# Optimization experiments

Measured on AMD Instinct MI355X. Metric: run time of the kernel, lower is better.

## Reference

```python
import jax, jax.numpy as jnp
import numpy as np
import math

N_NODES = 100000
N_EDGES = 1600000
IN_CH = 128
EDGE_DIM = 8
HEADS = 4
C1, C2 = 10, 5  # per-head out channels of conv1/conv2
N_GRAPHS = 64


def setup_inputs() -> dict:
    key = jax.random.key(0)
    k = jax.random.split(key, 26)
    s = 0.05
    d1, d2 = HEADS * C1, HEADS * C2  # 40, 20
    lin = lambda kk, fi, fo: jax.random.normal(kk, (fi, fo), jnp.float32) * s
    inp = {}
    inp['x'] = jax.random.normal(k[0], (N_NODES, IN_CH), jnp.float32)
    inp['edge_index'] = jax.random.randint(k[1], (2, N_EDGES), 0, N_NODES)
    inp['edge_attr'] = jax.random.normal(k[2], (N_EDGES, EDGE_DIM), jnp.float32)
    inp['batch'] = jnp.sort(jax.random.randint(k[3], (N_NODES,), 0, N_GRAPHS))
    # conv1 params (TransformerConv: lin_query/key/value + lin_edge(no bias) + lin_skip)
    inp['Wq1'] = lin(k[4], IN_CH, d1); inp['bq1'] = jnp.zeros((d1,), jnp.float32)
    inp['Wk1'] = lin(k[5], IN_CH, d1); inp['bk1'] = jnp.zeros((d1,), jnp.float32)
    inp['Wv1'] = lin(k[6], IN_CH, d1); inp['bv1'] = jnp.zeros((d1,), jnp.float32)
    inp['We1'] = lin(k[7], EDGE_DIM, d1)
    inp['Ws1'] = lin(k[8], IN_CH, d1); inp['bs1'] = jnp.zeros((d1,), jnp.float32)
    # conv2 params
    inp['Wq2'] = lin(k[9], d1, d2); inp['bq2'] = jnp.zeros((d2,), jnp.float32)
    inp['Wk2'] = lin(k[10], d1, d2); inp['bk2'] = jnp.zeros((d2,), jnp.float32)
    inp['Wv2'] = lin(k[11], d1, d2); inp['bv2'] = jnp.zeros((d2,), jnp.float32)
    inp['We2'] = lin(k[12], EDGE_DIM, d2)
    inp['Ws2'] = lin(k[13], d1, d2); inp['bs2'] = jnp.zeros((d2,), jnp.float32)
    # MLP head
    inp['W1'] = lin(k[14], d2, 10); inp['b1'] = jnp.zeros((10,), jnp.float32)
    inp['W2'] = lin(k[15], 10, 3); inp['b2'] = jnp.zeros((3,), jnp.float32)
    return inp


def _segment_softmax(alpha, dst, n):
    # numerically stable softmax over incoming edges of each target node
    amax = jax.ops.segment_max(alpha, dst, num_segments=n)
    ex = jnp.exp(alpha - amax[dst])
    den = jax.ops.segment_sum(ex, dst, num_segments=n)
    return ex / (den[dst] + 1e-16)


def _transformer_conv(x, src, dst, eattr, Wq, bq, Wk, bk, Wv, bv, We, Ws, bs, heads, ch):
    n = x.shape[0]
    q = (x @ Wq + bq).reshape(n, heads, ch)
    k = (x @ Wk + bk).reshape(n, heads, ch)
    v = (x @ Wv + bv).reshape(n, heads, ch)
    e = (eattr @ We).reshape(-1, heads, ch)          # [E,H,C]
    kj = k[src] + e                                   # gather + edge bias
    alpha = jnp.einsum('ehc,ehc->eh', q[dst], kj) / math.sqrt(ch)
    alpha = _segment_softmax(alpha, dst, n)           # [E,H]
    msg = (v[src] + e) * alpha[:, :, None]
    out = jax.ops.segment_sum(msg, dst, num_segments=n).reshape(n, heads * ch)
    return out + x @ Ws + bs                          # root/skip connection (beta=False)


def reference(x, edge_index, edge_attr, batch, Wq1, bq1, Wk1, bk1, Wv1, bv1, We1, Ws1, bs1, Wq2, bq2, Wk2, bk2, Wv2, bv2, We2, Ws2, bs2, W1, b1, W2, b2):
    src, dst = edge_index[0], edge_index[1]
    h = jax.nn.relu(_transformer_conv(x, src, dst, edge_attr, Wq1, bq1, Wk1, bk1, Wv1, bv1, We1, Ws1, bs1, HEADS, C1))
    h = jax.nn.relu(_transformer_conv(h, src, dst, edge_attr, Wq2, bq2, Wk2, bk2, Wv2, bv2, We2, Ws2, bs2, HEADS, C2))
    # global_mean_pool
    sums = jax.ops.segment_sum(h, batch, num_segments=N_GRAPHS)
    cnt = jax.ops.segment_sum(jnp.ones((h.shape[0],), h.dtype), batch, num_segments=N_GRAPHS)
    pooled = sums / jnp.maximum(cnt, 1.0)[:, None]
    h = jax.nn.relu(pooled @ W1 + b1)
    return h @ W2 + b2
```

## Files before the change

### kernel.cpp

```cpp
#include <hip/hip_runtime.h>
#include <math.h>

__device__ __forceinline__ unsigned bfr_(float f) {
    unsigned u = __float_as_uint(f);
    return (u + 0x7fffu + ((u >> 16) & 1u)) >> 16;
}
__device__ __forceinline__ unsigned pack2_(float lo, float hi) {
    return bfr_(lo) | (bfr_(hi) << 16);
}
__device__ __forceinline__ float unlo_(unsigned u) { return __uint_as_float(u << 16); }
__device__ __forceinline__ float unhi_(unsigned u) { return __uint_as_float(u & 0xffff0000u); }
__device__ __forceinline__ float bf2f_(unsigned short us) {
    return __uint_as_float((unsigned)us << 16);
}

__global__ void k_hist(const int* __restrict__ dst, int* __restrict__ deg, int E) {
    int e = blockIdx.x * 256 + threadIdx.x;
    if (e < E) atomicAdd(&deg[dst[e]], 1);
}

__global__ void k_scan1(const int* __restrict__ deg, int* __restrict__ rp,
                        int* __restrict__ bsum, int n) {
    __shared__ int sh[256];
    int t = threadIdx.x;
    int base = blockIdx.x * 1024 + t * 4;
    int v0 = (base + 0 < n) ? deg[base + 0] : 0;
    int v1 = (base + 1 < n) ? deg[base + 1] : 0;
    int v2 = (base + 2 < n) ? deg[base + 2] : 0;
    int v3 = (base + 3 < n) ? deg[base + 3] : 0;
    int ts = v0 + v1 + v2 + v3;
    sh[t] = ts;
    __syncthreads();
    for (int off = 1; off < 256; off <<= 1) {
        int x = (t >= off) ? sh[t - off] : 0;
        __syncthreads();
        sh[t] += x;
        __syncthreads();
    }
    int run = sh[t] - ts;
    if (base + 0 < n) rp[base + 0] = run;
    run += v0;
    if (base + 1 < n) rp[base + 1] = run;
    run += v1;
    if (base + 2 < n) rp[base + 2] = run;
    run += v2;
    if (base + 3 < n) rp[base + 3] = run;
    if (t == 255) bsum[blockIdx.x] = sh[255];
}

__global__ void k_scan2(int* __restrict__ bsum, int nb) {
    __shared__ int sh[256];
    int t = threadIdx.x;
    int v = (t < nb) ? bsum[t] : 0;
    sh[t] = v;
    __syncthreads();
    for (int off = 1; off < 256; off <<= 1) {
        int x = (t >= off) ? sh[t - off] : 0;
        __syncthreads();
        sh[t] += x;
        __syncthreads();
    }
    if (t < nb) bsum[t] = sh[t] - v;
}

__global__ void k_scan3(int* __restrict__ rp, const int* __restrict__ bsum,
                        int* __restrict__ cur, int n, int total) {
    int t = threadIdx.x;
    int base = blockIdx.x * 1024 + t * 4;
    int add = bsum[blockIdx.x];
    if (base + 0 < n) { rp[base + 0] += add; cur[base + 0] = 0; }
    if (base + 1 < n) { rp[base + 1] += add; cur[base + 1] = 0; }
    if (base + 2 < n) { rp[base + 2] += add; cur[base + 2] = 0; }
    if (base + 3 < n) { rp[base + 3] += add; cur[base + 3] = 0; }
    if (blockIdx.x == 0 && t == 0) rp[n] = total;
}

__global__ void k_scatter(const int* __restrict__ src, const int* __restrict__ dst,
                          const int* __restrict__ rp, int* __restrict__ cur,
                          const float4* __restrict__ ea, int* __restrict__ src_perm,
                          uint4* __restrict__ eap, int E) {
    int e = blockIdx.x * 256 + threadIdx.x;
    if (e >= E) return;
    float4 a = ea[(size_t)e * 2 + 0];
    float4 b = ea[(size_t)e * 2 + 1];
    uint4 u;
    u.x = pack2_(a.x, a.y);
    u.y = pack2_(a.z, a.w);
    u.z = pack2_(b.x, b.y);
    u.w = pack2_(b.z, b.w);
    int d = dst[e];
    int pos = rp[d] + atomicAdd(&cur[d], 1);
    src_perm[pos] = src[e];
    eap[pos] = u;
}

template <int FIN, int CH, int KTILE, int NPT, int CHPAD, int NPB>
__global__ __launch_bounds__(256) void k_proj(
    const float* __restrict__ X,
    const float* __restrict__ Wq, const float* __restrict__ Wk,
    const float* __restrict__ Wv, const float* __restrict__ Ws,
    const float* __restrict__ bq, const float* __restrict__ bk,
    const float* __restrict__ bv, const float* __restrict__ bs,
    float* __restrict__ qO, unsigned* __restrict__ kvO,
    unsigned short* __restrict__ sO, int N) {
    constexpr int FOUT = 4 * CH;
    constexpr int STRIDE = 4 * CHPAD;
    constexpr int COLS = 4 * FOUT;
    constexpr int NCG = COLS / 10;
    constexpr int NG = 256 / NCG;
    static_assert(NG * NPT == NPB, "geometry");
    constexpr int F4 = FIN / 4;
    __shared__ float xs[FIN * NPB];
    __shared__ float wbuf[KTILE * COLS];
    int t = threadIdx.x;
    int nb = blockIdx.x * NPB;
    for (int i = t; i < NPB * F4; i += 256) {
        int nl = i % NPB;
        int k4 = (i / NPB) * 4;
        int node = nb + nl;
        float4 val = make_float4(0.f, 0.f, 0.f, 0.f);
        if (node < N) val = *(const float4*)(X + (size_t)node * FIN + k4);
        xs[(k4 + 0) * NPB + nl] = val.x;
        xs[(k4 + 1) * NPB + nl] = val.y;
        xs[(k4 + 2) * NPB + nl] = val.z;
        xs[(k4 + 3) * NPB + nl] = val.w;
    }
    int cg = t % NCG, ng = t / NCG;
    int which = (cg * 10) / FOUT, cc0 = (cg * 10) % FOUT;
    float acc[NPT][10];
#pragma unroll
    for (int i = 0; i < NPT; ++i)
#pragma unroll
        for (int j = 0; j < 10; ++j) acc[i][j] = 0.f;

    for (int kt = 0; kt < FIN; kt += KTILE) {
        __syncthreads();
        for (int i = t; i < KTILE * (COLS / 4); i += 256) {
            int kk = i / (COLS / 4);
            int c4 = (i % (COLS / 4)) * 4;
            int wh = c4 / FOUT, cc = c4 % FOUT;
            const float* Wsrc = wh == 0 ? Wq : wh == 1 ? Wk : wh == 2 ? Wv : Ws;
            float4 wv = *(const float4*)(Wsrc + (size_t)(kt + kk) * FOUT + cc);
            wbuf[kk * COLS + c4 + 0] = wv.x;
            wbuf[kk * COLS + c4 + 1] = wv.y;
            wbuf[kk * COLS + c4 + 2] = wv.z;
            wbuf[kk * COLS + c4 + 3] = wv.w;
        }
        __syncthreads();
#pragma unroll 4
        for (int kk = 0; kk < KTILE; ++kk) {
            float xv[NPT];
            if constexpr (NPT == 4) {
                float4 x4 = *(const float4*)(xs + (kt + kk) * NPB + ng * 4);
                xv[0] = x4.x; xv[1] = x4.y; xv[2] = x4.z; xv[3] = x4.w;
            } else if constexpr (NPT == 2) {
                float2 x2 = *(const float2*)(xs + (kt + kk) * NPB + ng * 2);
                xv[0] = x2.x; xv[1] = x2.y;
            } else {
                xv[0] = xs[(kt + kk) * NPB + ng];
            }
            const float2* wp = (const float2*)(wbuf + kk * COLS + cg * 10);
            float wv[10];
#pragma unroll
            for (int jj = 0; jj < 5; ++jj) {
                float2 w2 = wp[jj];
                wv[2 * jj] = w2.x;
                wv[2 * jj + 1] = w2.y;
            }
#pragma unroll
            for (int i = 0; i < NPT; ++i)
#pragma unroll
                for (int j = 0; j < 10; ++j) acc[i][j] += xv[i] * wv[j];
        }
    }
    const float* B = which == 0 ? bq : which == 1 ? bk : which == 2 ? bv : bs;
    float bias[10];
#pragma unroll
    for (int j = 0; j < 10; ++j) bias[j] = B[cc0 + j];
    __syncthreads();
    if (which == 0) {
#pragma unroll
        for (int i = 0; i < NPT; ++i) {
            int node = nb + ng * NPT + i;
            if (node < N)
#pragma unroll
                for (int j = 0; j < 10; ++j) {
                    int col = cc0 + j, hh = col / CH, cc = col % CH;
                    qO[(size_t)node * STRIDE + hh * CHPAD + cc] = acc[i][j] + bias[j];
                }
        }
    } else if (which == 3) {
#pragma unroll
        for (int i = 0; i < NPT; ++i) {
            int node = nb + ng * NPT + i;
            if (node < N)
#pragma unroll
                for (int j = 0; j < 10; ++j)
                    sO[(size_t)node * FOUT + cc0 + j] =
                        (unsigned short)bfr_(acc[i][j] + bias[j]);
        }
    } else if (which == 1) {
#pragma unroll
        for (int i = 0; i < NPT; ++i) {
            int nl = ng * NPT + i;
#pragma unroll
            for (int j = 0; j < 10; ++j) wbuf[nl * FOUT + cc0 + j] = acc[i][j] + bias[j];
        }
    }
    __syncthreads();
    if (which == 2) {
#pragma unroll
        for (int i = 0; i < NPT; ++i) {
            int nl = ng * NPT + i;
            int node = nb + nl;
            if (node < N)
#pragma unroll
                for (int j = 0; j < 10; ++j) {
                    int col = cc0 + j, hh = col / CH, cc = col % CH;
                    float kf = wbuf[nl * FOUT + cc0 + j];
                    kvO[(size_t)node * STRIDE + hh * CHPAD + cc] =
                        pack2_(kf, acc[i][j] + bias[j]);
                }
        }
    }
}

template <int CH, int CHPAD, bool SHIFT>
__global__ __launch_bounds__(256) void k_conv(
    const int* __restrict__ rp, const int* __restrict__ src_perm,
    const uint4* __restrict__ eap, const float* __restrict__ We,
    const float* __restrict__ q, const unsigned* __restrict__ kv,
    const unsigned short* __restrict__ skp, float* __restrict__ hout,
    float inv_sqrt, int N) {
    constexpr int D = 4 * CH;
    constexpr int STRIDE = 4 * CHPAD;
    constexpr int RAWN = SHIFT ? CHPAD + 2 : CHPAD;
    constexpr int NLD = RAWN / 4;
    __shared__ float we_s[8 * D];
    for (int i = threadIdx.x; i < 8 * D; i += 256) we_s[i] = We[i];
    __syncthreads();
    int g = blockIdx.x * 256 + threadIdx.x;
    int node = g >> 4;
    int h = g & 3;
    int qtr = (g >> 2) & 3;
    if (node >= N) return;
    int start_off = SHIFT ? ((h * CH) & ~3) : h * CHPAD;
    int rs = rp[node], re = rp[node + 1];
    float qh[CH];
    {
        float qraw[RAWN];
        const float4* qp = (const float4*)(q + (size_t)node * STRIDE + start_off);
#pragma unroll
        for (int i = 0; i < NLD; ++i) *(float4*)&qraw[4 * i] = qp[i];
        if constexpr (SHIFT) {
            if (h & 1) {
#pragma unroll
                for (int c = 0; c < CH; ++c) qraw[c] = qraw[c + 2];
            }
        }
#pragma unroll
        for (int c = 0; c < CH; ++c) qh[c] = qraw[c];
    }
    float qe[8];
#pragma unroll
    for (int j = 0; j < 8; ++j) {
        float sE = 0.f;
#pragma unroll
        for (int c = 0; c < CH; ++c) sE += qh[c] * we_s[j * D + h * CH + c];
        qe[j] = sE;
    }
    float m = -3.0e38f, l = 0.f;
    float accv[CH] = {};
    float acce[8] = {};
    for (int p = rs + qtr; p < re; p += 4) {
        int sidx = src_perm[p];
        uint4 eu = eap[p];
        float ea8[8];
        ea8[0] = unlo_(eu.x); ea8[1] = unhi_(eu.x);
        ea8[2] = unlo_(eu.y); ea8[3] = unhi_(eu.y);
        ea8[4] = unlo_(eu.z); ea8[5] = unhi_(eu.z);
        ea8[6] = unlo_(eu.w); ea8[7] = unhi_(eu.w);
        unsigned kraw[RAWN];
        const uint4* kp = (const uint4*)(kv + (size_t)sidx * STRIDE + start_off);
#pragma unroll
        for (int i = 0; i < NLD; ++i) *(uint4*)&kraw[4 * i] = kp[i];
        if constexpr (SHIFT) {
            if (h & 1) {
#pragma unroll
                for (int c = 0; c < CH; ++c) kraw[c] = kraw[c + 2];
            }
        }
        float a = 0.f;
        float vj[CH];
#pragma unroll
        for (int c = 0; c < CH; ++c) {
            unsigned u = kraw[c];
            a += qh[c] * unlo_(u);
            vj[c] = unhi_(u);
        }
#pragma unroll
        for (int j = 0; j < 8; ++j) a += qe[j] * ea8[j];
        a *= inv_sqrt;
        float mn = fmaxf(m, a);
        float so = __expf(m - mn);
        float w = __expf(a - mn);
        l = l * so + w;
#pragma unroll
        for (int c = 0; c < CH; ++c) accv[c] = accv[c] * so + w * vj[c];
#pragma unroll
        for (int j = 0; j < 8; ++j) acce[j] = acce[j] * so + w * ea8[j];
        m = mn;
    }
#pragma unroll
    for (int mask = 4; mask <= 8; mask <<= 1) {
        float mo = __shfl_xor(m, mask);
        float lo = __shfl_xor(l, mask);
        float mn = fmaxf(m, mo);
        float s1 = (m > -1e37f) ? __expf(m - mn) : 0.f;
        float s2 = (mo > -1e37f) ? __expf(mo - mn) : 0.f;
        l = l * s1 + lo * s2;
#pragma unroll
        for (int c = 0; c < CH; ++c) {
            float ao = __shfl_xor(accv[c], mask);
            accv[c] = accv[c] * s1 + ao * s2;
        }
#pragma unroll
        for (int j = 0; j < 8; ++j) {
            float ao = __shfl_xor(acce[j], mask);
            acce[j] = acce[j] * s1 + ao * s2;
        }
        m = mn;
    }
    if (qtr == 0) {
        float inv = 1.0f / (l + 1e-16f);
#pragma unroll
        for (int c = 0; c < CH; ++c) {
            float ec = 0.f;
#pragma unroll
            for (int j = 0; j < 8; ++j) ec += acce[j] * we_s[j * D + h * CH + c];
            float o = (accv[c] + ec) * inv + bf2f_(skp[(size_t)node * D + h * CH + c]);
            hout[(size_t)node * D + h * CH + c] = fmaxf(o, 0.f);
        }
    }
}

__global__ void k_pool(const float* __restrict__ h2, const int* __restrict__ batch,
                       float* __restrict__ pooled, float* __restrict__ cnt, int N) {
    int t = blockIdx.x * 256 + threadIdx.x;
    int start = t * 16;
    if (start >= N) return;
    int end = min(start + 16, N);
    float acc[20];
#pragma unroll
    for (int c = 0; c < 20; ++c) acc[c] = 0.f;
    int cg = batch[start];
    float run = 0.f;
    for (int n = start; n < end; ++n) {
        int g = batch[n];
        if (g != cg) {
#pragma unroll
            for (int c = 0; c < 20; ++c) atomicAdd(&pooled[cg * 20 + c], acc[c]);
            atomicAdd(&cnt[cg], run);
#pragma unroll
            for (int c = 0; c < 20; ++c) acc[c] = 0.f;
            run = 0.f;
            cg = g;
        }
#pragma unroll
        for (int c = 0; c < 20; ++c) acc[c] += h2[(size_t)n * 20 + c];
        run += 1.f;
    }
#pragma unroll
    for (int c = 0; c < 20; ++c) atomicAdd(&pooled[cg * 20 + c], acc[c]);
    atomicAdd(&cnt[cg], run);
}

__global__ void k_mlp(const float* __restrict__ pooled, const float* __restrict__ cnt,
                      const float* __restrict__ W1, const float* __restrict__ b1,
                      const float* __restrict__ W2, const float* __restrict__ b2,
                      float* __restrict__ out) {
    int g = threadIdx.x;
    if (g >= 64) return;
    float ic = 1.0f / fmaxf(cnt[g], 1.0f);
    float p[20];
#pragma unroll
    for (int i = 0; i < 20; ++i) p[i] = pooled[g * 20 + i] * ic;
    float hid[10];
#pragma unroll
    for (int j = 0; j < 10; ++j) {
        float a = b1[j];
#pragma unroll
        for (int i = 0; i < 20; ++i) a += p[i] * W1[i * 10 + j];
        hid[j] = fmaxf(a, 0.f);
    }
#pragma unroll
    for (int o = 0; o < 3; ++o) {
        float a = b2[o];
#pragma unroll
        for (int j = 0; j < 10; ++j) a += hid[j] * W2[j * 3 + o];
        out[g * 3 + o] = a;
    }
}

extern "C" void kernel_launch(void* const* d_in, const int* in_sizes, int n_in,
                              void* d_out, int out_size, void* d_ws, size_t ws_size,
                              hipStream_t stream) {
    const float* x   = (const float*)d_in[0];
    const int* ei    = (const int*)d_in[1];
    const float* ea  = (const float*)d_in[2];
    const int* batch = (const int*)d_in[3];
    const float *Wq1 = (const float*)d_in[4],  *bq1 = (const float*)d_in[5];
    const float *Wk1 = (const float*)d_in[6],  *bk1 = (const float*)d_in[7];
    const float *Wv1 = (const float*)d_in[8],  *bv1 = (const float*)d_in[9];
    const float *We1 = (const float*)d_in[10];
    const float *Ws1 = (const float*)d_in[11], *bs1 = (const float*)d_in[12];
    const float *Wq2 = (const float*)d_in[13], *bq2 = (const float*)d_in[14];
    const float *Wk2 = (const float*)d_in[15], *bk2 = (const float*)d_in[16];
    const float *Wv2 = (const float*)d_in[17], *bv2 = (const float*)d_in[18];
    const float *We2 = (const float*)d_in[19];
    const float *Ws2 = (const float*)d_in[20], *bs2 = (const float*)d_in[21];
    const float *W1  = (const float*)d_in[22], *b1  = (const float*)d_in[23];
    const float *W2  = (const float*)d_in[24], *b2  = (const float*)d_in[25];

    const int N = in_sizes[0] / 128;
    const int E = in_sizes[1] / 2;
    const int* srcI = ei;
    const int* dstI = ei + E;

    float* F = (float*)d_ws;
    float*          q    = F;
    unsigned*       kv   = (unsigned*)(F + 4000000);
    float*          h1   = F + 8000000;
    float*          h2   = F + 8000000;
    unsigned short* s_bf = (unsigned short*)(F + 12000000);
    uint4*          eap  = (uint4*)(F + 14000000);
    int*       src_perm  = (int*)(F + 20400000);
    int* I = (int*)(F + 22000000);
    int* deg  = I;
    int* cur  = I;
    int* rpR  = I + 100352;
    int* bsum = I + 200704;
    float* pooled = F + 22300000;
    float* cnt    = pooled + 1280;

    const int SCAN_BLOCKS = (N + 1023) / 1024;
    const int EB = (E + 255) / 256;

    hipMemsetAsync(deg, 0, (size_t)N * 4, stream);
    hipMemsetAsync(pooled, 0, (1280 + 64) * 4, stream);

    k_hist<<<EB, 256, 0, stream>>>(dstI, deg, E);
    k_scan1<<<SCAN_BLOCKS, 256, 0, stream>>>(deg, rpR, bsum, N);
    k_scan2<<<1, 256, 0, stream>>>(bsum, SCAN_BLOCKS);
    k_scan3<<<SCAN_BLOCKS, 256, 0, stream>>>(rpR, bsum, cur, N, E);
    k_scatter<<<EB, 256, 0, stream>>>(srcI, dstI, rpR, cur, (const float4*)ea,
                                      src_perm, eap, E);

    k_proj<128, 10, 8, 4, 10, 64><<<(N + 63) / 64, 256, 0, stream>>>(
        x, Wq1, Wk1, Wv1, Ws1, bq1, bk1, bv1, bs1, q, kv, s_bf, N);
    k_conv<10, 10, true><<<(16 * N + 255) / 256, 256, 0, stream>>>(
        rpR, src_perm, eap, We1, q, kv, s_bf, h1, 0.31622776601683794f, N);

    k_proj<40, 5, 40, 1, 8, 32><<<(N + 31) / 32, 256, 0, stream>>>(
        h1, Wq2, Wk2, Wv2, Ws2, bq2, bk2, bv2, bs2, q, kv, s_bf, N);
    k_conv<5, 8, false><<<(16 * N + 255) / 256, 256, 0, stream>>>(
        rpR, src_perm, eap, We2, q, kv, s_bf, h2, 0.4472135954999579f, N);

    k_pool<<<((N + 15) / 16 + 255) / 256, 256, 0, stream>>>(h2, batch, pooled, cnt, N);
    k_mlp<<<1, 64, 0, stream>>>(pooled, cnt, W1, b1, W2, b2, (float*)d_out);
}
```

Measured before the change: 524.1 us.

## Split CSR scatter into bucketed staging pass and per-bucket local scatter

Replaces the single per-edge CSR scatter with two passes. The first pass uses one atomic counter per bucket of 16 destination nodes to write packed 64-bit records (local dst, edge id, src) into a staging buffer. The second pass runs one block per bucket, assigns final positions with shared-memory atomics, and writes src_perm and the bf16-packed edge attributes. The aim is to localize the random writes of the 16-byte edge-attribute records and cut global atomic contention, at the cost of an extra staging write/read and a gather of edge attributes by id. Bit packing assumes src < 2^17 and edge id < 2^21, and the staging buffer aliases the q buffer.

```diff
diff --git a/kernel.cpp b/kernel.cpp
--- a/kernel.cpp
+++ b/kernel.cpp
@@ -64,34 +64,64 @@
 }
 
 __global__ void k_scan3(int* __restrict__ rp, const int* __restrict__ bsum,
-                        int* __restrict__ cur, int n, int total) {
+                        int* __restrict__ bcur, int n, int total, int nbk) {
     int t = threadIdx.x;
     int base = blockIdx.x * 1024 + t * 4;
     int add = bsum[blockIdx.x];
-    if (base + 0 < n) { rp[base + 0] += add; cur[base + 0] = 0; }
-    if (base + 1 < n) { rp[base + 1] += add; cur[base + 1] = 0; }
-    if (base + 2 < n) { rp[base + 2] += add; cur[base + 2] = 0; }
-    if (base + 3 < n) { rp[base + 3] += add; cur[base + 3] = 0; }
+    if (base + 0 < n) rp[base + 0] += add;
+    if (base + 1 < n) rp[base + 1] += add;
+    if (base + 2 < n) rp[base + 2] += add;
+    if (base + 3 < n) rp[base + 3] += add;
+    int gid = blockIdx.x * 256 + t;
+    if (gid < nbk) bcur[gid] = 0;
     if (blockIdx.x == 0 && t == 0) rp[n] = total;
 }
 
-__global__ void k_scatter(const int* __restrict__ src, const int* __restrict__ dst,
-                          const int* __restrict__ rp, int* __restrict__ cur,
-                          const float4* __restrict__ ea, int* __restrict__ src_perm,
-                          uint4* __restrict__ eap, int E) {
+__global__ void k_scatterB(const int* __restrict__ src, const int* __restrict__ dst,
+                           const int* __restrict__ rp, int* __restrict__ bcur,
+                           unsigned long long* __restrict__ staging, int E) {
     int e = blockIdx.x * 256 + threadIdx.x;
     if (e >= E) return;
-    float4 a = ea[(size_t)e * 2 + 0];
-    float4 b = ea[(size_t)e * 2 + 1];
-    uint4 u;
-    u.x = pack2_(a.x, a.y);
-    u.y = pack2_(a.z, a.w);
-    u.z = pack2_(b.x, b.y);
-    u.w = pack2_(b.z, b.w);
     int d = dst[e];
-    int pos = rp[d] + atomicAdd(&cur[d], 1);
-    src_perm[pos] = src[e];
-    eap[pos] = u;
+    int b = d >> 4;
+    int pos = rp[d & ~15] + atomicAdd(&bcur[b], 1);
+    unsigned long long rec = ((unsigned long long)(d & 15) << 38) |
+                             ((unsigned long long)(unsigned)e << 17) |
+                             (unsigned long long)(unsigned)src[e];
+    staging[pos] = rec;
+}
+
+__global__ __launch_bounds__(256) void k_scatterC(
+    const int* __restrict__ rp, const unsigned long long* __restrict__ staging,
+    const float4* __restrict__ ea, int* __restrict__ src_perm,
+    uint4* __restrict__ eap, int N, int nbk) {
+    __shared__ int lcur[16];
+    __shared__ int rpl[17];
+    int b = blockIdx.x;
+    int t = threadIdx.x;
+    int node0 = b << 4;
+    if (t < 16) lcur[t] = 0;
+    if (t < 17) rpl[t] = rp[min(node0 + t, N)];
+    __syncthreads();
+    int start = rpl[0];
+    int cnt = rpl[16] - start;
+    for (int i = t; i < cnt; i += 256) {
+        unsigned long long rec = staging[start + i];
+        int dl = (int)(rec >> 38);
+        int eid = (int)((rec >> 17) & 0x1FFFFFu);
+        int srcv = (int)(rec & 0x1FFFFu);
+        int idx = atomicAdd(&lcur[dl], 1);
+        int fin = rpl[dl] + idx;
+        src_perm[fin] = srcv;
+        float4 a = ea[(size_t)eid * 2 + 0];
+        float4 bb = ea[(size_t)eid * 2 + 1];
+        uint4 u;
+        u.x = pack2_(a.x, a.y);
+        u.y = pack2_(a.z, a.w);
+        u.z = pack2_(bb.x, bb.y);
+        u.w = pack2_(bb.z, bb.w);
+        eap[fin] = u;
+    }
 }
 
 template <int FIN, int CH, int KTILE, int NPT, int CHPAD, int NPB>
@@ -435,16 +465,18 @@
     unsigned short* s_bf = (unsigned short*)(F + 12000000);
     uint4*          eap  = (uint4*)(F + 14000000);
     int*       src_perm  = (int*)(F + 20400000);
+    unsigned long long* staging = (unsigned long long*)F;
     int* I = (int*)(F + 22000000);
     int* deg  = I;
-    int* cur  = I;
     int* rpR  = I + 100352;
     int* bsum = I + 200704;
+    int* bcur = I + 200960;
     float* pooled = F + 22300000;
     float* cnt    = pooled + 1280;
 
     const int SCAN_BLOCKS = (N + 1023) / 1024;
     const int EB = (E + 255) / 256;
+    const int NBK = (N + 15) >> 4;
 
     hipMemsetAsync(deg, 0, (size_t)N * 4, stream);
     hipMemsetAsync(pooled, 0, (1280 + 64) * 4, stream);
@@ -452,9 +484,10 @@
     k_hist<<<EB, 256, 0, stream>>>(dstI, deg, E);
     k_scan1<<<SCAN_BLOCKS, 256, 0, stream>>>(deg, rpR, bsum, N);
     k_scan2<<<1, 256, 0, stream>>>(bsum, SCAN_BLOCKS);
-    k_scan3<<<SCAN_BLOCKS, 256, 0, stream>>>(rpR, bsum, cur, N, E);
-    k_scatter<<<EB, 256, 0, stream>>>(srcI, dstI, rpR, cur, (const float4*)ea,
-                                      src_perm, eap, E);
+    k_scan3<<<SCAN_BLOCKS, 256, 0, stream>>>(rpR, bsum, bcur, N, E, NBK);
+    k_scatterB<<<EB, 256, 0, stream>>>(srcI, dstI, rpR, bcur, staging, E);
+    k_scatterC<<<NBK, 256, 0, stream>>>(rpR, staging, (const float4*)ea,
+                                        src_perm, eap, N, NBK);
 
     k_proj<128, 10, 8, 4, 10, 64><<<(N + 63) / 64, 256, 0, stream>>>(
         x, Wq1, Wk1, Wv1, Ws1, bq1, bk1, bv1, bs1, q, kv, s_bf, N);
```

New measurement: 539.3 us. +2.9%, slower.

## Use bf16 MFMA for first-layer QKV/skip projection with prepacked weights

Applied to the files above, without the earlier changes.

Replaces the scalar FMA projection for conv1 with a kernel that converts X tiles to bf16 in LDS and computes all four projections (160 columns) with 16x16x32 bf16 MFMA instructions. A small prep kernel transposes and packs the weights to bf16 with padded rows once per call. The aim is to cut the compute cost of the 128-input projection over 100k nodes. In exchange, inputs and weights are rounded to bf16 before accumulation, which lowers precision, and the kernel uses about 60KB of LDS, which may limit occupancy.

```diff
diff --git a/kernel.cpp b/kernel.cpp
--- a/kernel.cpp
+++ b/kernel.cpp
@@ -1,5 +1,8 @@
 #include <hip/hip_runtime.h>
 #include <math.h>
+
+typedef short bf16x8 __attribute__((ext_vector_type(8)));
+typedef float f32x4 __attribute__((ext_vector_type(4)));
 
 __device__ __forceinline__ unsigned bfr_(float f) {
     unsigned u = __float_as_uint(f);
@@ -92,6 +95,92 @@
     int pos = rp[d] + atomicAdd(&cur[d], 1);
     src_perm[pos] = src[e];
     eap[pos] = u;
+}
+
+__global__ void k_wprep(const float* __restrict__ Wq, const float* __restrict__ Wk,
+                        const float* __restrict__ Wv, const float* __restrict__ Ws,
+                        short* __restrict__ wpackT) {
+    int i = blockIdx.x * 256 + threadIdx.x;
+    if (i >= 160 * 136) return;
+    int c = i / 136, k = i % 136;
+    short v = 0;
+    if (k < 128) {
+        const float* W = c < 40 ? Wq : c < 80 ? Wk : c < 120 ? Wv : Ws;
+        v = (short)bfr_(W[k * 40 + (c % 40)]);
+    }
+    wpackT[i] = v;
+}
+
+__global__ __launch_bounds__(256) void k_proj1m(
+    const float* __restrict__ X, const short* __restrict__ wpackT,
+    const float* __restrict__ bq, const float* __restrict__ bk,
+    const float* __restrict__ bv, const float* __restrict__ bs,
+    float* __restrict__ qO, unsigned* __restrict__ kvO,
+    unsigned short* __restrict__ sO, int N) {
+    __shared__ short xs[64 * 136];
+    __shared__ short wt[160 * 136];
+    int t = threadIdx.x;
+    int nb = blockIdx.x * 64;
+    for (int i = t; i < 64 * 32; i += 256) {
+        int nl = i >> 5, k4 = (i & 31) * 4;
+        int node = nb + nl;
+        float4 val = make_float4(0.f, 0.f, 0.f, 0.f);
+        if (node < N) val = *(const float4*)(X + (size_t)node * 128 + k4);
+        uint2 pk;
+        pk.x = pack2_(val.x, val.y);
+        pk.y = pack2_(val.z, val.w);
+        *(uint2*)(xs + nl * 136 + k4) = pk;
+    }
+    {
+        const uint4* wsrc = (const uint4*)wpackT;
+        uint4* wdst = (uint4*)wt;
+        for (int i = t; i < 2720; i += 256) wdst[i] = wsrc[i];
+    }
+    __syncthreads();
+    int wv = t >> 6;
+    int lane = t & 63;
+    int lrow = lane & 15;
+    int kgrp = lane >> 4;
+    bf16x8 afr[4];
+    const short* xbase = xs + (wv * 16 + lrow) * 136;
+#pragma unroll
+    for (int kk = 0; kk < 4; ++kk)
+        afr[kk] = *(const bf16x8*)(xbase + kk * 32 + kgrp * 8);
+    f32x4 acc[10];
+#pragma unroll
+    for (int nt = 0; nt < 10; ++nt) acc[nt] = (f32x4){0.f, 0.f, 0.f, 0.f};
+#pragma unroll
+    for (int nt = 0; nt < 10; ++nt) {
+        const short* wbase = wt + (nt * 16 + lrow) * 136;
+#pragma unroll
+        for (int kk = 0; kk < 4; ++kk) {
+            bf16x8 bfr8 = *(const bf16x8*)(wbase + kk * 32 + kgrp * 8);
+            acc[nt] = __builtin_amdgcn_mfma_f32_16x16x32_bf16(afr[kk], bfr8, acc[nt],
+                                                              0, 0, 0);
+        }
+    }
+    __syncthreads();
+    float* cs = (float*)wt;
+#pragma unroll
+    for (int nt = 0; nt < 10; ++nt)
+#pragma unroll
+        for (int r = 0; r < 4; ++r)
+            cs[(wv * 16 + kgrp * 4 + r) * 160 + nt * 16 + lrow] = acc[nt][r];
+    __syncthreads();
+    for (int i = t; i < 64 * 40; i += 256) {
+        int nl = i / 40, c = i % 40;
+        int node = nb + nl;
+        if (node < N) {
+            const float* row = cs + nl * 160;
+            float qv = row[c] + bq[c];
+            float kf = row[40 + c] + bk[c];
+            float vf = row[80 + c] + bv[c];
+            float sv = row[120 + c] + bs[c];
+            qO[(size_t)node * 40 + c] = qv;
+            kvO[(size_t)node * 40 + c] = pack2_(kf, vf);
+            sO[(size_t)node * 40 + c] = (unsigned short)bfr_(sv);
+        }
+    }
 }
 
 template <int FIN, int CH, int KTILE, int NPT, int CHPAD, int NPB>
@@ -440,6 +529,7 @@
     int* cur  = I;
     int* rpR  = I + 100352;
     int* bsum = I + 200704;
+    short* wpackT = (short*)(F + 22250000);
     float* pooled = F + 22300000;
     float* cnt    = pooled + 1280;
 
@@ -449,6 +539,7 @@
     hipMemsetAsync(deg, 0, (size_t)N * 4, stream);
     hipMemsetAsync(pooled, 0, (1280 + 64) * 4, stream);
 
+    k_wprep<<<(160 * 136 + 255) / 256, 256, 0, stream>>>(Wq1, Wk1, Wv1, Ws1, wpackT);
     k_hist<<<EB, 256, 0, stream>>>(dstI, deg, E);
     k_scan1<<<SCAN_BLOCKS, 256, 0, stream>>>(deg, rpR, bsum, N);
     k_scan2<<<1, 256, 0, stream>>>(bsum, SCAN_BLOCKS);
@@ -456,8 +547,8 @@
     k_scatter<<<EB, 256, 0, stream>>>(srcI, dstI, rpR, cur, (const float4*)ea,
                                       src_perm, eap, E);
 
-    k_proj<128, 10, 8, 4, 10, 64><<<(N + 63) / 64, 256, 0, stream>>>(
-        x, Wq1, Wk1, Wv1, Ws1, bq1, bk1, bv1, bs1, q, kv, s_bf, N);
+    k_proj1m<<<(N + 63) / 64, 256, 0, stream>>>(x, wpackT, bq1, bk1, bv1, bs1,
+                                                q, kv, s_bf, N);
     k_conv<10, 10, true><<<(16 * N + 255) / 256, 256, 0, stream>>>(
         rpR, src_perm, eap, We1, q, kv, s_bf, h1, 0.31622776601683794f, N);
 
```

Result: faster. 475.2 us (-9.3%).
